# Performance work log

Hardware: AMD Instinct MI355X
Metric: run time of the kernel (lower is better)

Reference implementation:

```python
import jax, jax.numpy as jnp
import numpy as np

B, S, H = 2, 1024, 4096
NH, NKV, D = 32, 8, 128
N_REP = NH // NKV
SCALE = D ** -0.5
ROPE_BASE = 1000000.0
NEG_INF = -1e9


def _rope_tables(dtype=jnp.float32):
    inv_freq = 1.0 / (ROPE_BASE ** (jnp.arange(0, D, 2, dtype=jnp.float32) / D))
    pos = jnp.arange(S, dtype=jnp.float32)
    freqs = pos[:, None] * inv_freq[None, :]              # [S, D/2]
    emb = jnp.concatenate([freqs, freqs], axis=-1)        # [S, D]
    cos = jnp.broadcast_to(jnp.cos(emb)[None], (B, S, D)).astype(dtype)
    sin = jnp.broadcast_to(jnp.sin(emb)[None], (B, S, D)).astype(dtype)
    return cos, sin


def setup_inputs() -> dict:
    key = jax.random.key(0)
    k1, k2, k3, k4, k5 = jax.random.split(key, 5)
    hidden_states = jax.random.normal(k1, (B, S, H), dtype=jnp.float32)
    # weights stored as [in, out] so application is x @ W
    Wq = jax.random.normal(k2, (H, NH * D), dtype=jnp.float32) * (H ** -0.5)
    Wk = jax.random.normal(k3, (H, NKV * D), dtype=jnp.float32) * (H ** -0.5)
    Wv = jax.random.normal(k4, (H, NKV * D), dtype=jnp.float32) * (H ** -0.5)
    Wo = jax.random.normal(k5, (NH * D, H), dtype=jnp.float32) * ((NH * D) ** -0.5)
    cos, sin = _rope_tables()
    causal = jnp.tril(jnp.ones((S, S), dtype=bool))
    attention_mask = jnp.where(causal, 0.0, NEG_INF).astype(jnp.float32)
    attention_mask = jnp.broadcast_to(attention_mask[None, None], (B, 1, S, S))
    return {"hidden_states": hidden_states, "cos": cos, "sin": sin,
            "attention_mask": attention_mask, "Wq": Wq, "Wk": Wk, "Wv": Wv, "Wo": Wo}


def _rotate_half(x):
    x1, x2 = x[..., : D // 2], x[..., D // 2:]
    return jnp.concatenate([-x2, x1], axis=-1)


def reference(hidden_states, cos, sin, attention_mask, Wq, Wk, Wv, Wo):
    # projections -> [B, heads, S, D]
    q = (hidden_states @ Wq).reshape(B, S, NH, D).transpose(0, 2, 1, 3)
    k = (hidden_states @ Wk).reshape(B, S, NKV, D).transpose(0, 2, 1, 3)
    v = (hidden_states @ Wv).reshape(B, S, NKV, D).transpose(0, 2, 1, 3)
    # RoPE (cos/sin unsqueezed over head dim)
    c = cos[:, None, :, :]
    s = sin[:, None, :, :]
    q = q * c + _rotate_half(q) * s
    k = k * c + _rotate_half(k) * s
    # repeat_kv for GQA
    k = jnp.repeat(k, N_REP, axis=1)   # [B, NH, S, D]
    v = jnp.repeat(v, N_REP, axis=1)
    scores = jnp.einsum('bhqd,bhkd->bhqk', q, k) * SCALE + attention_mask
    weights = jax.nn.softmax(scores.astype(jnp.float32), axis=-1).astype(q.dtype)
    attn = jnp.einsum('bhqk,bhkd->bhqd', weights, v)
    attn = attn.transpose(0, 2, 1, 3).reshape(B, S, NH * D)
    return attn @ Wo
```

## Files before the change

kernel.cpp:

```cpp
#include <hip/hip_runtime.h>

typedef unsigned short u16;
typedef __bf16 bf16x8 __attribute__((ext_vector_type(8)));
typedef float f32x4 __attribute__((ext_vector_type(4)));

#define SCALE_QK 0.08838834764831845f
#define LOG2E 1.4426950408889634f
#define NEGBIG (-1e9f)

static __device__ __forceinline__ float bf2f(u16 u) {
  union { float f; unsigned int i; } x; x.i = ((unsigned int)u) << 16; return x.f;
}
static __device__ __forceinline__ u16 f2bf(float f) {
  union { float f; unsigned int i; } x; x.f = f;
  return (u16)((x.i + 0x7fffu + ((x.i >> 16) & 1u)) >> 16);
}
static __device__ __forceinline__ void async16(const u16* g, u16* s) {
  __builtin_amdgcn_global_load_lds(
      (const __attribute__((address_space(1))) void*)g,
      (__attribute__((address_space(3))) void*)s, 16, 0, 0);
}

__global__ __launch_bounds__(64) void detect_dtype(
    const void* p0, const void* p1, const void* p2, const void* p3,
    const void* p4, const void* p5, int* flags) {
  const void* ps[6] = {p0, p1, p2, p3, p4, p5};
  const u16* p = (const u16*)ps[blockIdx.x];
  int lane = threadIdx.x;
  u16 u = p[2 * lane];
  int e = (u >> 7) & 0xFF;
  int plaus = (e >= 112 && e <= 143) ? 1 : 0;
  unsigned long long m = __ballot(plaus);
  if (lane == 0) {
    flags[blockIdx.x] = (__popcll(m) < 32) ? 1 : 0;
    if (blockIdx.x == 0) flags[6] = 0;
  }
}

static __device__ __forceinline__ void transpose_body(
    const void* __restrict__ src, u16* __restrict__ dst, int N, int K,
    int n0, int k0, int f32in, u16* t) {
  const int LT = 74;
  const int tid = threadIdx.x;
  for (int c = tid; c < 512; c += 256) {
    int r = c >> 3, ch = (c & 7) * 8;
    u16* tp = t + r * LT + ch;
    if (f32in) {
      const float* p = (const float*)src + (size_t)(k0 + r) * N + n0 + ch;
      float4 v0 = *(const float4*)p;
      float4 v1 = *(const float4*)(p + 4);
      tp[0] = f2bf(v0.x); tp[1] = f2bf(v0.y); tp[2] = f2bf(v0.z); tp[3] = f2bf(v0.w);
      tp[4] = f2bf(v1.x); tp[5] = f2bf(v1.y); tp[6] = f2bf(v1.z); tp[7] = f2bf(v1.w);
    } else {
      uint4 v = *(const uint4*)((const u16*)src + (size_t)(k0 + r) * N + n0 + ch);
      const u16* pv = (const u16*)&v;
#pragma unroll
      for (int e = 0; e < 8; ++e) tp[e] = pv[e];
    }
  }
  __syncthreads();
  for (int c = tid; c < 512; c += 256) {
    int rr = c >> 3, cc = (c & 7) * 8;
    u16 tmp[8];
#pragma unroll
    for (int e = 0; e < 8; ++e) tmp[e] = t[(cc + e) * LT + rr];
    *(uint4*)(dst + (size_t)(n0 + rr) * K + k0 + cc) = *(const uint4*)tmp;
  }
}

__global__ __launch_bounds__(256) void transpose_to_bf16(
    const void* __restrict__ src, u16* __restrict__ dst, int N, int K,
    const int* __restrict__ flag) {
  __shared__ u16 t[64 * 74];
  transpose_body(src, dst, N, K, blockIdx.x * 64, blockIdx.y * 64, *flag, t);
}

__global__ __launch_bounds__(256) void prep_fused(
    const void* __restrict__ Wq, const void* __restrict__ Wk,
    const void* __restrict__ Wv, u16* __restrict__ dst,
    const void* __restrict__ hidden, u16* __restrict__ Xb,
    const int* __restrict__ flags) {
  __shared__ u16 t[64 * 74];
  int bx = blockIdx.x;
  if (bx < 96) {
    const void* src; u16* d; int N; int f32in; int nx;
    if (bx < 64)      { src = Wq; d = dst;                       N = 4096; f32in = flags[2]; nx = bx; }
    else if (bx < 80) { src = Wk; d = dst + (size_t)4096 * 4096; N = 1024; f32in = flags[3]; nx = bx - 64; }
    else              { src = Wv; d = dst + (size_t)5120 * 4096; N = 1024; f32in = flags[4]; nx = bx - 80; }
    transpose_body(src, d, N, 4096, nx * 64, blockIdx.y * 64, f32in, t);
  } else {
    int i = (((bx - 96) * 64 + blockIdx.y) * 256 + threadIdx.x) * 8;
    if (flags[0]) {
      float4 v0 = *(const float4*)((const float*)hidden + i);
      float4 v1 = *(const float4*)((const float*)hidden + i + 4);
      u16 tmp[8] = {f2bf(v0.x), f2bf(v0.y), f2bf(v0.z), f2bf(v0.w),
                    f2bf(v1.x), f2bf(v1.y), f2bf(v1.z), f2bf(v1.w)};
      *(uint4*)(Xb + i) = *(const uint4*)tmp;
    } else {
      *(uint4*)(Xb + i) = *(const uint4*)((const u16*)hidden + i);
    }
  }
}

template <int BM, int BN, int NWM, int NWN>
__global__ __launch_bounds__(512, 2) void gemm_ph(
    const u16* __restrict__ A, const u16* __restrict__ Bt, void* __restrict__ C,
    int K, int lda, int ldb, int ldc, const int* __restrict__ oflag) {
  constexpr int AL = BM / 128, BL = BN / 128, L = AL + BL;
  constexpr int HALF = (BM + BN) * 32;
  constexpr int WM = BM / NWM, WN = BN / NWN;
  constexpr int FM = WM / 16, FN = WN / 16;
  __shared__ u16 lds[HALF * 4];
  const int tid = threadIdx.x;
  const int wave = tid >> 6, lane = tid & 63;
  const int quad = lane >> 4, l16 = lane & 15;
  const int wr = wave / NWN, wc = wave % NWN;

  const int nwg = gridDim.x * gridDim.y;
  const int flat = blockIdx.y * gridDim.x + blockIdx.x;
  const int swz = (flat & 7) * (nwg >> 3) + (flat >> 3);
  const int bm = (swz % gridDim.y) * BM;
  const int bn = (swz / gridDim.y) * BN;
  const int f32out = *oflag;

  int rA[AL], kA[AL], rB[BL], kB[BL];
#pragma unroll
  for (int i = 0; i < AL; ++i) {
    int c = i * 512 + tid; rA[i] = c >> 2;
    kA[i] = ((c & 3) ^ ((rA[i] >> 1) & 3)) * 8;
  }
#pragma unroll
  for (int i = 0; i < BL; ++i) {
    int c = i * 512 + tid; rB[i] = c >> 2;
    kB[i] = ((c & 3) ^ ((rB[i] >> 1) & 3)) * 8;
  }
  const int H = K >> 5;

  const int ch = (quad ^ ((l16 >> 1) & 3)) * 8;

  auto STAGE = [&](int hh) {
    u16* dst = lds + (hh & 3) * HALF;
#pragma unroll
    for (int i = 0; i < AL; ++i)
      async16(A + (size_t)(bm + rA[i]) * lda + hh * 32 + kA[i],
              dst + (i * 512 + tid) * 8);
#pragma unroll
    for (int i = 0; i < BL; ++i)
      async16(Bt + (size_t)(bn + rB[i]) * ldb + hh * 32 + kB[i],
              dst + BM * 32 + (i * 512 + tid) * 8);
  };

  f32x4 acc[FM][FN] = {};

  STAGE(0); STAGE(1); STAGE(2);
  if constexpr (L == 4) { asm volatile("s_waitcnt vmcnt(8)" ::: "memory"); }
  else                  { asm volatile("s_waitcnt vmcnt(6)" ::: "memory"); }
  asm volatile("s_barrier" ::: "memory");

  for (int hh = 0; hh < H; ++hh) {
    const u16* bufA = lds + (hh & 3) * HALF;
    const u16* bufB = bufA + BM * 32;
    bf16x8 af[FM], bv[FN];
#pragma unroll
    for (int mi = 0; mi < FM; ++mi)
      af[mi] = *(const bf16x8*)(bufA + (wr * WM + mi * 16 + l16) * 32 + ch);
#pragma unroll
    for (int ni = 0; ni < FN; ++ni)
      bv[ni] = *(const bf16x8*)(bufB + (wc * WN + ni * 16 + l16) * 32 + ch);
    if (hh + 3 < H) STAGE(hh + 3);
    asm volatile("s_waitcnt lgkmcnt(0)" ::: "memory");
    __builtin_amdgcn_sched_barrier(0);
    __builtin_amdgcn_s_setprio(1);
#pragma unroll
    for (int mi = 0; mi < FM; ++mi)
#pragma unroll
      for (int ni = 0; ni < FN; ++ni)
        acc[mi][ni] = __builtin_amdgcn_mfma_f32_16x16x32_bf16(
            af[mi], bv[ni], acc[mi][ni], 0, 0, 0);
    __builtin_amdgcn_s_setprio(0);
    if (hh + 3 < H) {
      if constexpr (L == 4) { asm volatile("s_waitcnt vmcnt(8)" ::: "memory"); }
      else                  { asm volatile("s_waitcnt vmcnt(6)" ::: "memory"); }
    } else if (hh + 2 < H) {
      if constexpr (L == 4) { asm volatile("s_waitcnt vmcnt(4)" ::: "memory"); }
      else                  { asm volatile("s_waitcnt vmcnt(3)" ::: "memory"); }
    } else if (hh + 1 < H) {
      asm volatile("s_waitcnt vmcnt(0)" ::: "memory");
    }
    asm volatile("s_barrier" ::: "memory");
  }

#pragma unroll
  for (int mi = 0; mi < FM; ++mi) {
    int row = bm + wr * WM + mi * 16 + quad * 4;
#pragma unroll
    for (int ni = 0; ni < FN; ++ni) {
      int col = bn + wc * WN + ni * 16 + l16;
#pragma unroll
      for (int r = 0; r < 4; ++r) {
        size_t idx = (size_t)(row + r) * ldc + col;
        if (f32out) ((float*)C)[idx] = acc[mi][ni][r];
        else ((u16*)C)[idx] = f2bf(acc[mi][ni][r]);
      }
    }
  }
}

__global__ __launch_bounds__(256) void rope_kernel(
    u16* __restrict__ QKV, const void* __restrict__ cosb,
    const void* __restrict__ sinb, const int* __restrict__ flag) {
  int idx = blockIdx.x * 256 + threadIdx.x;
  int d8 = (idx & 7) * 8;
  int rest = idx >> 3;
  int slot = rest % 40;
  int tok = rest / 40;
  int col = (slot < 32) ? (slot * 128 + d8) : (4096 + (slot - 32) * 128 + d8);
  size_t base = (size_t)tok * 6144 + col;
  uint4 va = *(const uint4*)(QKV + base);
  uint4 vb = *(const uint4*)(QKV + base + 64);
  const u16* pa = (const u16*)&va;
  const u16* pb = (const u16*)&vb;
  size_t cb = (size_t)tok * 128 + d8;
  float c1[8], s1[8], c2[8], s2[8];
  if (*flag) {
    const float* cp = (const float*)cosb + cb;
    const float* sp = (const float*)sinb + cb;
    float4 t0 = *(const float4*)cp,        t1 = *(const float4*)(cp + 4);
    float4 t2 = *(const float4*)(cp + 64), t3 = *(const float4*)(cp + 68);
    float4 u0 = *(const float4*)sp,        u1 = *(const float4*)(sp + 4);
    float4 u2 = *(const float4*)(sp + 64), u3 = *(const float4*)(sp + 68);
    c1[0]=t0.x;c1[1]=t0.y;c1[2]=t0.z;c1[3]=t0.w;c1[4]=t1.x;c1[5]=t1.y;c1[6]=t1.z;c1[7]=t1.w;
    c2[0]=t2.x;c2[1]=t2.y;c2[2]=t2.z;c2[3]=t2.w;c2[4]=t3.x;c2[5]=t3.y;c2[6]=t3.z;c2[7]=t3.w;
    s1[0]=u0.x;s1[1]=u0.y;s1[2]=u0.z;s1[3]=u0.w;s1[4]=u1.x;s1[5]=u1.y;s1[6]=u1.z;s1[7]=u1.w;
    s2[0]=u2.x;s2[1]=u2.y;s2[2]=u2.z;s2[3]=u2.w;s2[4]=u3.x;s2[5]=u3.y;s2[6]=u3.z;s2[7]=u3.w;
  } else {
    const u16* cp = (const u16*)cosb + cb;
    const u16* sp = (const u16*)sinb + cb;
    uint4 t0 = *(const uint4*)cp, t1 = *(const uint4*)(cp + 64);
    uint4 u0 = *(const uint4*)sp, u1 = *(const uint4*)(sp + 64);
    const u16* q0 = (const u16*)&t0; const u16* q1 = (const u16*)&t1;
    const u16* r0 = (const u16*)&u0; const u16* r1 = (const u16*)&u1;
#pragma unroll
    for (int e = 0; e < 8; ++e) {
      c1[e] = bf2f(q0[e]); c2[e] = bf2f(q1[e]);
      s1[e] = bf2f(r0[e]); s2[e] = bf2f(r1[e]);
    }
  }
  u16 o1[8], o2[8];
#pragma unroll
  for (int e = 0; e < 8; ++e) {
    float x1 = bf2f(pa[e]), x2 = bf2f(pb[e]);
    o1[e] = f2bf(x1 * c1[e] - x2 * s1[e]);
    o2[e] = f2bf(x2 * c2[e] + x1 * s2[e]);
  }
  *(uint4*)(QKV + base) = *(const uint4*)o1;
  *(uint4*)(QKV + base + 64) = *(const uint4*)o2;
}

__global__ __launch_bounds__(256, 3) void attn_kernel(
    const u16* __restrict__ QKV, u16* __restrict__ O) {
  const int LK = 136;
  const int LP = 72;
  __shared__ u16 sK[64 * LK];
  __shared__ u16 sV[128 * 64];
  __shared__ u16 sP[64 * LP];
  const int tid = threadIdx.x, wave = tid >> 6, lane = tid & 63;
  const int quad = lane >> 4, l16 = lane & 15;
  const int pp = blockIdx.x, h = blockIdx.y, b = blockIdx.z;
  const int kvh = h >> 2;
  const size_t tb = (size_t)b * 1024 * 6144;
  const u16* Qg = QKV + tb + (size_t)h * 128;
  const u16* Kg = QKV + tb + 4096 + (size_t)kvh * 128;
  const u16* Vg = QKV + tb + 5120 + (size_t)kvh * 128;

#pragma unroll 1
  for (int pass = 0; pass < 2; ++pass) {
    const int qt = pass ? (15 - pp) : pp;

    bf16x8 qa[4];
    {
      const int qrow = qt * 64 + wave * 16 + l16;
#pragma unroll
      for (int kc = 0; kc < 4; ++kc) {
        bf16x8 v = *(const bf16x8*)(Qg + (size_t)qrow * 6144 + kc * 32 + quad * 8);
#pragma unroll
        for (int e = 0; e < 8; ++e) v[e] = (__bf16)((float)v[e] * (SCALE_QK * LOG2E));
        qa[kc] = v;
      }
    }

    uint4 kreg[4], vreg[4];
#pragma unroll
    for (int i = 0; i < 4; ++i) {
      int c = i * 256 + tid, row = c >> 4, ch = (c & 15) * 8;
      kreg[i] = *(const uint4*)(Kg + (size_t)row * 6144 + ch);
      vreg[i] = *(const uint4*)(Vg + (size_t)row * 6144 + ch);
    }

    float m_run = -INFINITY, l_run = 0.f;
    f32x4 oacc[8] = {};
    const int qg = qt * 64 + wave * 16 + l16;

    const int nkb = qt + 1;
    for (int kb = 0; kb < nkb; ++kb) {
#pragma unroll
      for (int i = 0; i < 4; ++i) {
        int c = i * 256 + tid, row = c >> 4, ch = (c & 15) * 8;
        *(uint4*)(sK + row * LK + ch) = kreg[i];
        const u16* pw = (const u16*)&vreg[i];
#pragma unroll
        for (int e = 0; e < 8; ++e) {
          int d = ch + e;
          sV[d * 64 + ((((row >> 3) ^ (d >> 3)) & 7) << 3) + (row & 7)] = pw[e];
        }
      }
      __syncthreads();
      if (kb + 1 < nkb) {
#pragma unroll
        for (int i = 0; i < 4; ++i) {
          int c = i * 256 + tid, row = c >> 4, ch = (c & 15) * 8;
          kreg[i] = *(const uint4*)(Kg + (size_t)((kb + 1) * 64 + row) * 6144 + ch);
          vreg[i] = *(const uint4*)(Vg + (size_t)((kb + 1) * 64 + row) * 6144 + ch);
        }
      }

      f32x4 st[4] = {};
#pragma unroll
      for (int kc = 0; kc < 4; ++kc)
#pragma unroll
        for (int j = 0; j < 4; ++j) {
          bf16x8 bb = *(const bf16x8*)(sK + (j * 16 + l16) * LK + kc * 32 + quad * 8);
          st[j] = __builtin_amdgcn_mfma_f32_16x16x32_bf16(bb, qa[kc], st[j], 0, 0, 0);
        }

      const int kg0 = kb * 64 + quad * 4;
      float mloc = NEGBIG;
#pragma unroll
      for (int j = 0; j < 4; ++j)
#pragma unroll
        for (int r = 0; r < 4; ++r) {
          float v = st[j][r];
          if (kg0 + j * 16 + r > qg) v = NEGBIG;
          st[j][r] = v;
          mloc = fmaxf(mloc, v);
        }
      mloc = fmaxf(mloc, __shfl_xor(mloc, 16, 64));
      mloc = fmaxf(mloc, __shfl_xor(mloc, 32, 64));

      if (__any(mloc - m_run > 8.0f)) {
        float mn = fmaxf(m_run, mloc);
        float alpha = exp2f(m_run - mn);
        m_run = mn;
        l_run *= alpha;
        float ar[4];
#pragma unroll
        for (int r = 0; r < 4; ++r) ar[r] = __shfl(alpha, quad * 4 + r, 64);
#pragma unroll
        for (int dt = 0; dt < 8; ++dt)
#pragma unroll
          for (int r = 0; r < 4; ++r) oacc[dt][r] *= ar[r];
      }

      float lad = 0.f;
#pragma unroll
      for (int j = 0; j < 4; ++j)
#pragma unroll
        for (int r = 0; r < 4; ++r) {
          float p = exp2f(st[j][r] - m_run);
          st[j][r] = p;
          lad += p;
        }
      lad += __shfl_xor(lad, 16, 64);
      lad += __shfl_xor(lad, 32, 64);
      l_run += lad;

#pragma unroll
      for (int j = 0; j < 4; ++j)
#pragma unroll
        for (int r = 0; r < 4; ++r)
          sP[(wave * 16 + l16) * LP + j * 16 + quad * 4 + r] = f2bf(st[j][r]);
      __asm__ __volatile__("s_waitcnt lgkmcnt(0)" ::: "memory");

#pragma unroll
      for (int kc = 0; kc < 2; ++kc) {
        bf16x8 a = *(const bf16x8*)(sP + (wave * 16 + l16) * LP + kc * 32 + quad * 8);
#pragma unroll
        for (int dt = 0; dt < 8; ++dt) {
          int d = dt * 16 + l16;
          int chk = ((kc * 4 + quad) ^ (d >> 3)) & 7;
          bf16x8 bb = *(const bf16x8*)(sV + d * 64 + chk * 8);
          oacc[dt] = __builtin_amdgcn_mfma_f32_16x16x32_bf16(a, bb, oacc[dt], 0, 0, 0);
        }
      }
      __syncthreads();
    }

    float lfin[4];
#pragma unroll
    for (int r = 0; r < 4; ++r) lfin[r] = __shfl(l_run, quad * 4 + r, 64);

    const int srow = qt * 64 + wave * 16 + quad * 4;
#pragma unroll
    for (int dt = 0; dt < 8; ++dt)
#pragma unroll
      for (int r = 0; r < 4; ++r) {
        float val = oacc[dt][r] / lfin[r];
        O[((size_t)b * 1024 + srow + r) * 4096 + h * 128 + dt * 16 + l16] = f2bf(val);
      }
  }
}

extern "C" void kernel_launch(void* const* d_in, const int* in_sizes, int n_in,
                              void* d_out, int out_size, void* d_ws, size_t ws_size,
                              hipStream_t stream) {
  (void)in_sizes; (void)n_in; (void)out_size; (void)ws_size;
  const void* hidden = d_in[0];
  const void* cosb   = d_in[1];
  const void* sinb   = d_in[2];
  const void* Wq = d_in[4];
  const void* Wk = d_in[5];
  const void* Wv = d_in[6];
  const void* Wo = d_in[7];

  u16* ws = (u16*)d_ws;
  u16* Wqkvt = ws;
  u16* Wot   = ws;
  u16* Xb    = ws + (size_t)25165824;
  u16* attnb = Xb;
  u16* QKV   = ws + (size_t)33554432;
  int* flags = (int*)(ws + (size_t)46137344);

  detect_dtype<<<6, 64, 0, stream>>>(hidden, cosb, Wq, Wk, Wv, Wo, flags);

  prep_fused<<<dim3(160, 64), 256, 0, stream>>>(Wq, Wk, Wv, Wqkvt, hidden, Xb, flags);

  gemm_ph<256, 256, 2, 4><<<dim3(24, 8), 512, 0, stream>>>(
      Xb, Wqkvt, QKV, 4096, 4096, 4096, 6144, flags + 6);
  rope_kernel<<<2560, 256, 0, stream>>>(QKV, cosb, sinb, flags + 1);

  transpose_to_bf16<<<dim3(64, 64), 256, 0, stream>>>(Wo, Wot, 4096, 4096, flags + 5);

  attn_kernel<<<dim3(8, 32, 2), 256, 0, stream>>>(QKV, attnb);

  gemm_ph<256, 128, 4, 2><<<dim3(32, 8), 512, 0, stream>>>(
      attnb, Wot, d_out, 4096, 4096, 4096, 4096, flags + 0);
}
```

Baseline: 471.1 us.

## Rewrite GEMM mainloop as 8-phase half-tile pipeline with 64-wide K stages

```diff
diff --git a/kernel.cpp b/kernel.cpp
--- a/kernel.cpp
+++ b/kernel.cpp
@@ -103,14 +103,17 @@
 }
 
 template <int BM, int BN, int NWM, int NWN>
-__global__ __launch_bounds__(512, 2) void gemm_ph(
+__global__ __launch_bounds__(512, 2) void gemm_8ph(
     const u16* __restrict__ A, const u16* __restrict__ Bt, void* __restrict__ C,
     int K, int lda, int ldb, int ldc, const int* __restrict__ oflag) {
-  constexpr int AL = BM / 128, BL = BN / 128, L = AL + BL;
-  constexpr int HALF = (BM + BN) * 32;
   constexpr int WM = BM / NWM, WN = BN / NWN;
   constexpr int FM = WM / 16, FN = WN / 16;
-  __shared__ u16 lds[HALF * 4];
+  constexpr int FMH = FM / 2, FNH = FN / 2;
+  constexpr int BHALF = BN / 2;
+  constexpr int AU = 128 * 64;
+  constexpr int BU = BHALF * 64;
+  constexpr int BLD = BU / (512 * 8);
+  __shared__ u16 lds[(AU + BU) * 4];
   const int tid = threadIdx.x;
   const int wave = tid >> 6, lane = tid & 63;
   const int quad = lane >> 4, l16 = lane & 15;
@@ -122,72 +125,108 @@
   const int bm = (swz % gridDim.y) * BM;
   const int bn = (swz / gridDim.y) * BN;
   const int f32out = *oflag;
-
-  int rA[AL], kA[AL], rB[BL], kB[BL];
-#pragma unroll
-  for (int i = 0; i < AL; ++i) {
-    int c = i * 512 + tid; rA[i] = c >> 2;
-    kA[i] = ((c & 3) ^ ((rA[i] >> 1) & 3)) * 8;
-  }
-#pragma unroll
-  for (int i = 0; i < BL; ++i) {
-    int c = i * 512 + tid; rB[i] = c >> 2;
-    kB[i] = ((c & 3) ^ ((rB[i] >> 1) & 3)) * 8;
-  }
-  const int H = K >> 5;
-
-  const int ch = (quad ^ ((l16 >> 1) & 3)) * 8;
-
-  auto STAGE = [&](int hh) {
-    u16* dst = lds + (hh & 3) * HALF;
-#pragma unroll
-    for (int i = 0; i < AL; ++i)
-      async16(A + (size_t)(bm + rA[i]) * lda + hh * 32 + kA[i],
-              dst + (i * 512 + tid) * 8);
-#pragma unroll
-    for (int i = 0; i < BL; ++i)
-      async16(Bt + (size_t)(bn + rB[i]) * ldb + hh * 32 + kB[i],
-              dst + BM * 32 + (i * 512 + tid) * 8);
+  const int NK = K >> 6;
+
+  constexpr int UO[8] = {0, AU, AU + BU, AU + 2 * BU,
+                         2 * AU + 2 * BU, 3 * AU + 2 * BU,
+                         3 * AU + 3 * BU, 3 * AU + 4 * BU};
+
+  const int arow0 = wr * WM;
+  const int brow0 = wc * WN;
+
+  auto stage = [&](int u, int kt) {
+    if (kt >= NK) return;
+    u16* base = lds + UO[u];
+    int us = u & 3;
+    if (us == 0 || us == 3) {
+      int mh = (us == 3);
+#pragma unroll
+      for (int c0 = 0; c0 < 2; ++c0) {
+        int c = c0 * 512 + tid;
+        int row = bm + mh * 128 + (c >> 3);
+        int col = kt * 64 + ((c & 7) ^ ((c >> 3) & 7)) * 8;
+        async16(A + (size_t)row * lda + col, base + c * 8);
+      }
+    } else {
+      int nh = (us == 2);
+#pragma unroll
+      for (int c0 = 0; c0 < BLD; ++c0) {
+        int c = c0 * 512 + tid;
+        int row = bn + nh * BHALF + (c >> 3);
+        int col = kt * 64 + ((c & 7) ^ ((c >> 3) & 7)) * 8;
+        async16(Bt + (size_t)row * ldb + col, base + c * 8);
+      }
+    }
   };
 
   f32x4 acc[FM][FN] = {};
-
-  STAGE(0); STAGE(1); STAGE(2);
-  if constexpr (L == 4) { asm volatile("s_waitcnt vmcnt(8)" ::: "memory"); }
-  else                  { asm volatile("s_waitcnt vmcnt(6)" ::: "memory"); }
+  bf16x8 af[FMH][2];
+  bf16x8 bvh[2][FNH][2];
+
+  stage(0, 0); stage(1, 0); stage(2, 0); stage(3, 0);
+  stage(5, 1); stage(6, 1);
+  if constexpr (BLD == 2) { asm volatile("s_waitcnt vmcnt(4)" ::: "memory"); }
+  else                    { asm volatile("s_waitcnt vmcnt(2)" ::: "memory"); }
   asm volatile("s_barrier" ::: "memory");
 
-  for (int hh = 0; hh < H; ++hh) {
-    const u16* bufA = lds + (hh & 3) * HALF;
-    const u16* bufB = bufA + BM * 32;
-    bf16x8 af[FM], bv[FN];
-#pragma unroll
-    for (int mi = 0; mi < FM; ++mi)
-      af[mi] = *(const bf16x8*)(bufA + (wr * WM + mi * 16 + l16) * 32 + ch);
-#pragma unroll
-    for (int ni = 0; ni < FN; ++ni)
-      bv[ni] = *(const bf16x8*)(bufB + (wc * WN + ni * 16 + l16) * 32 + ch);
-    if (hh + 3 < H) STAGE(hh + 3);
-    asm volatile("s_waitcnt lgkmcnt(0)" ::: "memory");
-    __builtin_amdgcn_sched_barrier(0);
-    __builtin_amdgcn_s_setprio(1);
-#pragma unroll
-    for (int mi = 0; mi < FM; ++mi)
-#pragma unroll
-      for (int ni = 0; ni < FN; ++ni)
-        acc[mi][ni] = __builtin_amdgcn_mfma_f32_16x16x32_bf16(
-            af[mi], bv[ni], acc[mi][ni], 0, 0, 0);
-    __builtin_amdgcn_s_setprio(0);
-    if (hh + 3 < H) {
-      if constexpr (L == 4) { asm volatile("s_waitcnt vmcnt(8)" ::: "memory"); }
-      else                  { asm volatile("s_waitcnt vmcnt(6)" ::: "memory"); }
-    } else if (hh + 2 < H) {
-      if constexpr (L == 4) { asm volatile("s_waitcnt vmcnt(4)" ::: "memory"); }
-      else                  { asm volatile("s_waitcnt vmcnt(3)" ::: "memory"); }
-    } else if (hh + 1 < H) {
-      asm volatile("s_waitcnt vmcnt(0)" ::: "memory");
-    }
-    asm volatile("s_barrier" ::: "memory");
+  constexpr int SU[8]  = {4, 7, 1, 2, 0, 3, 5, 6};
+  constexpr int SKT[8] = {1, 1, 2, 2, 2, 2, 3, 3};
+
+  const int IT = NK >> 1;
+#pragma unroll 1
+  for (int it = 0; it < IT; ++it) {
+#pragma unroll
+    for (int p = 0; p < 8; ++p) {
+      const int kt = p >> 2, sub = p & 3;
+      const int mh = sub >> 1, nh = sub & 1;
+      if (sub == 0 || sub == 2) {
+        const int r0 = arow0 + mh * (WM / 2);
+        const u16* abase = lds + UO[kt * 4 + ((r0 >> 7) ? 3 : 0)];
+        const int lr0 = r0 & 127;
+#pragma unroll
+        for (int mi = 0; mi < FMH; ++mi) {
+          const int lr = lr0 + mi * 16 + l16;
+#pragma unroll
+          for (int ks = 0; ks < 2; ++ks)
+            af[mi][ks] = *(const bf16x8*)(
+                abase + lr * 64 + (((ks * 4 + quad) ^ (lr & 7)) * 8));
+        }
+      }
+      if (sub == 0 || sub == 1) {
+        const int c0 = brow0 + nh * FNH * 16;
+        const u16* bbase = lds + UO[kt * 4 + 1 + (c0 / BHALF)];
+        const int lc0 = c0 % BHALF;
+#pragma unroll
+        for (int ni = 0; ni < FNH; ++ni) {
+          const int lr = lc0 + ni * 16 + l16;
+#pragma unroll
+          for (int ks = 0; ks < 2; ++ks)
+            bvh[nh][ni][ks] = *(const bf16x8*)(
+                bbase + lr * 64 + (((ks * 4 + quad) ^ (lr & 7)) * 8));
+        }
+      }
+      stage(SU[p], 2 * it + SKT[p]);
+      if (sub == 0 && FM == 8)
+        asm volatile("s_waitcnt lgkmcnt(8)" ::: "memory");
+      asm volatile("s_barrier" ::: "memory");
+      asm volatile("s_waitcnt lgkmcnt(0)" ::: "memory");
+      __builtin_amdgcn_sched_barrier(0);
+      __builtin_amdgcn_s_setprio(1);
+#pragma unroll
+      for (int mi = 0; mi < FMH; ++mi)
+#pragma unroll
+        for (int ni = 0; ni < FNH; ++ni) {
+          f32x4* a = &acc[mh * FMH + mi][nh * FNH + ni];
+          *a = __builtin_amdgcn_mfma_f32_16x16x32_bf16(af[mi][0], bvh[nh][ni][0], *a, 0, 0, 0);
+          *a = __builtin_amdgcn_mfma_f32_16x16x32_bf16(af[mi][1], bvh[nh][ni][1], *a, 0, 0, 0);
+        }
+      __builtin_amdgcn_s_setprio(0);
+      if (p == 3 || p == 7) {
+        if constexpr (BLD == 2) { asm volatile("s_waitcnt vmcnt(4)" ::: "memory"); }
+        else                    { asm volatile("s_waitcnt vmcnt(2)" ::: "memory"); }
+      }
+      asm volatile("s_barrier" ::: "memory");
+    }
   }
 
 #pragma unroll
@@ -434,7 +473,7 @@
 
   prep_fused<<<dim3(160, 64), 256, 0, stream>>>(Wq, Wk, Wv, Wqkvt, hidden, Xb, flags);
 
-  gemm_ph<256, 256, 2, 4><<<dim3(24, 8), 512, 0, stream>>>(
+  gemm_8ph<256, 256, 2, 4><<<dim3(24, 8), 512, 0, stream>>>(
       Xb, Wqkvt, QKV, 4096, 4096, 4096, 6144, flags + 6);
   rope_kernel<<<2560, 256, 0, stream>>>(QKV, cosb, sinb, flags + 1);
 
@@ -442,6 +481,6 @@
 
   attn_kernel<<<dim3(8, 32, 2), 256, 0, stream>>>(QKV, attnb);
 
-  gemm_ph<256, 128, 4, 2><<<dim3(32, 8), 512, 0, stream>>>(
+  gemm_8ph<256, 128, 4, 2><<<dim3(32, 8), 512, 0, stream>>>(
       attnb, Wot, d_out, 4096, 4096, 4096, 4096, flags + 0);
 }
```

After: 483.7 us. 2.7% more time.
